# Optimization experiments

Measured on AMD Instinct MI355X. Metric: run time of the kernel, lower is better.

Reference implementation:

```python
import jax, jax.numpy as jnp
import numpy as np

N = 8192       # nodes per graph
E = 262144     # edges per graph (avg degree 32)
H = 8          # attention heads
C = 128        # hidden dim per head (H*C = 1024 to match Linear(1024,128))
IN = 128       # input feature dim
NEG_SLOPE = 0.2


def _gat_conv(x, edge_index, W, att_src, att_dst, bias):
    """PyG GATConv (concat=True, add_self_loops=True, shared lin for src/dst)."""
    n = x.shape[0]
    loop = jnp.arange(n, dtype=edge_index.dtype)
    src = jnp.concatenate([edge_index[0], loop])  # [E+N]
    dst = jnp.concatenate([edge_index[1], loop])
    h = (x @ W).reshape(n, H, C)                         # [N,H,C]
    a_src = jnp.sum(h * att_src, axis=-1)                # [N,H]
    a_dst = jnp.sum(h * att_dst, axis=-1)                # [N,H]
    e = jax.nn.leaky_relu(a_src[src] + a_dst[dst], NEG_SLOPE)   # [E+N,H]
    m = jax.ops.segment_max(e, dst, num_segments=n)      # per-dst max for stability
    ex = jnp.exp(e - m[dst])
    den = jax.ops.segment_sum(ex, dst, num_segments=n)
    alpha = ex / den[dst]                                # [E+N,H] neighborhood softmax
    out = jax.ops.segment_sum(h[src] * alpha[:, :, None], dst, num_segments=n)
    return out.reshape(n, H * C) + bias                  # [N, H*C]


def setup_inputs() -> dict:
    key = jax.random.key(0)
    ks = jax.random.split(key, 12)
    s = 0.05  # keep activations in a sane range
    return {
        "x1": jax.random.normal(ks[0], (N, IN), jnp.float32),
        "edge_index1": jax.random.randint(ks[1], (2, E), 0, N, dtype=jnp.int64),
        "W1": jax.random.normal(ks[2], (IN, H * C), jnp.float32) * s,
        "att_src1": jax.random.normal(ks[3], (H, C), jnp.float32) * s,
        "att_dst1": jax.random.normal(ks[4], (H, C), jnp.float32) * s,
        "b1": jnp.zeros((H * C,), jnp.float32),
        "x2": jax.random.normal(ks[5], (N, IN), jnp.float32),
        "edge_index2": jax.random.randint(ks[6], (2, E), 0, N, dtype=jnp.int64),
        "W2": jax.random.normal(ks[7], (IN, H * C), jnp.float32) * s,
        "att_src2": jax.random.normal(ks[8], (H, C), jnp.float32) * s,
        "att_dst2": jax.random.normal(ks[9], (H, C), jnp.float32) * s,
        "b2": jnp.zeros((H * C,), jnp.float32),
        "Wl": jax.random.normal(ks[10], (H * C, 128), jnp.float32) * s,
        "bl": jnp.zeros((128,), jnp.float32),
    }


def reference(x1, edge_index1, W1, att_src1, att_dst1, b1,
              x2, edge_index2, W2, att_src2, att_dst2, b2, Wl, bl):
    emb1 = _gat_conv(x1, edge_index1, W1, att_src1, att_dst1, b1)  # [N1,1024]
    emb2 = _gat_conv(x2, edge_index2, W2, att_src2, att_dst2, b2)  # [N2,1024]
    scores = emb1 @ emb2.T                                          # [N1,N2]
    w1 = jax.nn.softmax(scores, axis=1)
    w2 = jax.nn.softmax(scores, axis=0)
    cross1 = (w2 @ emb2) @ Wl + bl      # [N1,128]
    cross2 = (w1.T @ emb1) @ Wl + bl    # [N2,128]
    return (jnp.mean(cross1, axis=0), jnp.mean(cross2, axis=0))
```

## Files before the change

### kernel.cpp

```cpp
#include <hip/hip_runtime.h>


#define NN 8192
#define EE 262144
#define NEG 0.2f

#define BKT 128
#define RNG (NN / BKT)
#define CAP 2560
#define EB  128
#define CHK (EE / EB)

#define U_CNT   0
#define U_G     (U_CNT + 4*BKT)
#define U_MEMB  (U_G + 2048)
#define U_ZEND  (U_MEMB + 2048)
#define U_U     (U_ZEND)
#define U_ASRC  (U_U + 2*2048)
#define U_ADST  (U_ASRC + 2*NN*8)
#define U_PR    (U_ADST + 2*NN*8)
#define U_WACC  (U_PR + 2*NN*16)
#define U_BIND  (U_WACC + 2*NN*8)
#define U_BINS  (U_BIND + 2*BKT*CAP)
#define ZERO_BYTES ((size_t)U_ZEND * 4)

__global__ __launch_bounds__(256) void k_u(
    const float* __restrict__ W1, const float* __restrict__ as1, const float* __restrict__ ad1,
    const float* __restrict__ W2, const float* __restrict__ as2, const float* __restrict__ ad2,
    float* __restrict__ u) {
  int b = blockIdx.x;
  int graph = b >> 4, sd = (b >> 3) & 1, head = b & 7;
  const float* W = graph ? W2 : W1;
  const float* att = graph ? (sd ? ad2 : as2) : (sd ? ad1 : as1);
  int w = threadIdx.x >> 6, lane = threadIdx.x & 63;
  float2 av = ((const float2*)(att + head * 128))[lane];
  float* uo = u + graph * 2048 + sd * 1024 + head * 128;
#pragma unroll 4
  for (int k = w; k < 128; k += 4) {
    float2 wv = ((const float2*)(W + (size_t)k * 1024 + head * 128))[lane];
    float p = av.x * wv.x + av.y * wv.y;
    p += __shfl_xor(p, 1);  p += __shfl_xor(p, 2);  p += __shfl_xor(p, 4);
    p += __shfl_xor(p, 8);  p += __shfl_xor(p, 16); p += __shfl_xor(p, 32);
    if (lane == 0) uo[k] = p;
  }
}

__global__ __launch_bounds__(256) void k_a(
    const float* __restrict__ x1, const float* __restrict__ x2,
    const float* __restrict__ u, float* __restrict__ asrc, float* __restrict__ adst) {
  int graph = blockIdx.y;
  const float* x = graph ? x2 : x1;
  const float* ug = u + graph * 2048;
  __shared__ float xs[64][129];
  __shared__ float us[16][128];
  int t = threadIdx.x;
  for (int i = t; i < 2048; i += 256) us[i >> 7][i & 127] = ug[i];
  int n0 = blockIdx.x * 64;
  const float* xb = x + (size_t)n0 * 128;
  for (int i = t; i < 64 * 128; i += 256) xs[i >> 7][i & 127] = xb[i];
  __syncthreads();
  int nl = t & 63;
  int j0 = (t >> 6) * 4;
  float a0 = 0.f, a1 = 0.f, a2 = 0.f, a3 = 0.f;
#pragma unroll 4
  for (int k = 0; k < 128; ++k) {
    float xv = xs[nl][k];
    a0 += xv * us[j0 + 0][k];
    a1 += xv * us[j0 + 1][k];
    a2 += xv * us[j0 + 2][k];
    a3 += xv * us[j0 + 3][k];
  }
  int n = n0 + nl;
  float* outp = (j0 < 8) ? (asrc + graph * (NN * 8) + n * 8 + j0)
                         : (adst + graph * (NN * 8) + n * 8 + (j0 - 8));
  outp[0] = a0; outp[1] = a1; outp[2] = a2; outp[3] = a3;
}

__global__ __launch_bounds__(512) void k_bin(
    const int* __restrict__ ei1, const int* __restrict__ ei2,
    int* __restrict__ cnt, int* __restrict__ binD, int* __restrict__ binS) {
  int g = blockIdx.y;
  const int* ei = g ? ei2 : ei1;
  __shared__ int hD[BKT], hS[BKT], bD[BKT], bS[BKT], cD[BKT], cS[BKT];
  int t = threadIdx.x;
  for (int i = t; i < BKT; i += 512) { hD[i] = 0; hS[i] = 0; cD[i] = 0; cS[i] = 0; }
  __syncthreads();
  int e0 = blockIdx.x * CHK;
  for (int i = t; i < CHK; i += 512) {
    int s = ei[e0 + i], d = ei[EE + e0 + i];
    atomicAdd(&hD[d >> 6], 1);
    atomicAdd(&hS[s >> 6], 1);
  }
  __syncthreads();
  for (int i = t; i < BKT; i += 512) {
    bD[i] = atomicAdd(cnt + (2 * g + 0) * BKT + i, hD[i]);
    bS[i] = atomicAdd(cnt + (2 * g + 1) * BKT + i, hS[i]);
  }
  __syncthreads();
  int* bdg = binD + (size_t)g * BKT * CAP;
  int* bsg = binS + (size_t)g * BKT * CAP;
  for (int i = t; i < CHK; i += 512) {
    int s = ei[e0 + i], d = ei[EE + e0 + i];
    int kb = d >> 6;
    int p = bD[kb] + atomicAdd(&cD[kb], 1);
    bdg[kb * CAP + p] = (s << 6) | (d & 63);
    kb = s >> 6;
    p = bS[kb] + atomicAdd(&cS[kb], 1);
    bsg[kb * CAP + p] = (d << 6) | (s & 63);
  }
}

__global__ __launch_bounds__(512) void k_den_red(
    const int* __restrict__ cnt, const int* __restrict__ binD,
    const float* __restrict__ asrc, const float* __restrict__ adst,
    float* __restrict__ pr) {
  int g = blockIdx.y, b = blockIdx.x;
  int lo = b * RNG;
  const float* as = asrc + g * (NN * 8);
  const float* ad = adst + g * (NN * 8);
  float2* prg = (float2*)pr + (size_t)g * (NN * 8);
  __shared__ float den[RNG * 8];
  __shared__ float adsts[RNG * 8];
  int t = threadIdx.x;
  for (int i = t; i < RNG * 8; i += 512) {
    float avv = ad[lo * 8 + i];
    float v = as[lo * 8 + i] + avv;
    v = v > 0.f ? v : NEG * v;
    adsts[i] = avv;
    den[i] = __expf(v);
  }
  __syncthreads();
  int n = cnt[(2 * g + 0) * BKT + b];
  const int* recs = binD + (size_t)g * BKT * CAP + b * CAP;
  int rid = t >> 3, h = t & 7;
  for (int base = 0; base < n; base += 256) {
    int rv[4]; bool ok[4]; float sv[4];
#pragma unroll
    for (int uu = 0; uu < 4; ++uu) {
      int i = base + uu * 64 + rid;
      ok[uu] = i < n;
      rv[uu] = ok[uu] ? recs[i] : 0;
    }
#pragma unroll
    for (int uu = 0; uu < 4; ++uu)
      sv[uu] = ok[uu] ? as[(rv[uu] >> 6) * 8 + h] : 0.f;
#pragma unroll
    for (int uu = 0; uu < 4; ++uu) {
      if (ok[uu]) {
        int dl = rv[uu] & 63;
        float v = sv[uu] + adsts[dl * 8 + h];
        v = v > 0.f ? v : NEG * v;
        atomicAdd(&den[dl * 8 + h], __expf(v));
      }
    }
  }
  __syncthreads();
  for (int i = t; i < RNG * 8; i += 512)
    prg[lo * 8 + i] = make_float2(adsts[i], 1.0f / den[i]);
}

__global__ __launch_bounds__(512) void k_wacc_red(
    const int* __restrict__ cnt, const int* __restrict__ binS,
    const float* __restrict__ asrc, const float* __restrict__ pr,
    float* __restrict__ wacc) {
  int g = blockIdx.y, b = blockIdx.x;
  int lo = b * RNG;
  const float* as = asrc + g * (NN * 8);
  const float2* prg = (const float2*)pr + (size_t)g * (NN * 8);
  __shared__ float wv[RNG * 8];
  __shared__ float asrcs[RNG * 8];
  int t = threadIdx.x;
  for (int i = t; i < RNG * 8; i += 512) {
    float sva = as[lo * 8 + i];
    float2 f2 = prg[lo * 8 + i];
    float v = sva + f2.x;
    v = v > 0.f ? v : NEG * v;
    asrcs[i] = sva;
    wv[i] = __expf(v) * f2.y;
  }
  __syncthreads();
  int n = cnt[(2 * g + 1) * BKT + b];
  const int* recs = binS + (size_t)g * BKT * CAP + b * CAP;
  int rid = t >> 3, h = t & 7;
  for (int base = 0; base < n; base += 256) {
    int rv[4]; bool ok[4]; float2 pv[4];
#pragma unroll
    for (int uu = 0; uu < 4; ++uu) {
      int i = base + uu * 64 + rid;
      ok[uu] = i < n;
      rv[uu] = ok[uu] ? recs[i] : 0;
    }
#pragma unroll
    for (int uu = 0; uu < 4; ++uu)
      pv[uu] = ok[uu] ? prg[(size_t)(rv[uu] >> 6) * 8 + h] : make_float2(0.f, 0.f);
#pragma unroll
    for (int uu = 0; uu < 4; ++uu) {
      if (ok[uu]) {
        int sl = rv[uu] & 63;
        float v = asrcs[sl * 8 + h] + pv[uu].x;
        v = v > 0.f ? v : NEG * v;
        atomicAdd(&wv[sl * 8 + h], __expf(v) * pv[uu].y);
      }
    }
  }
  __syncthreads();
  for (int i = t; i < RNG * 8; i += 512)
    wacc[g * (NN * 8) + lo * 8 + i] = wv[i];
}

#define GCHUNK 128
__global__ __launch_bounds__(256) void k_gred(
    const float* __restrict__ x1, const float* __restrict__ x2,
    const float* __restrict__ wacc, float* __restrict__ g) {
  int graph = blockIdx.y;
  const float* x = graph ? x2 : x1;
  const float* w = wacc + graph * (NN * 8);
  float* gg = g + graph * 1024;
  int t = threadIdx.x;
  int k = t & 127;
  int h0 = (t >> 7) * 4;
  int n0 = blockIdx.x * GCHUNK;
  float a0 = 0.f, a1 = 0.f, a2 = 0.f, a3 = 0.f;
#pragma unroll 4
  for (int n = n0; n < n0 + GCHUNK; ++n) {
    float xv = x[(size_t)n * 128 + k];
    float4 wv4 = *(const float4*)(w + (size_t)n * 8 + h0);
    a0 += xv * wv4.x; a1 += xv * wv4.y; a2 += xv * wv4.z; a3 += xv * wv4.w;
  }
  atomicAdd(gg + (h0 + 0) * 128 + k, a0);
  atomicAdd(gg + (h0 + 1) * 128 + k, a1);
  atomicAdd(gg + (h0 + 2) * 128 + k, a2);
  atomicAdd(gg + (h0 + 3) * 128 + k, a3);
}

__global__ __launch_bounds__(256) void k_memb(
    const float* __restrict__ W1, const float* __restrict__ W2,
    const float* __restrict__ b1, const float* __restrict__ b2,
    const float* __restrict__ g, float* __restrict__ memb) {
  int graph = blockIdx.z;
  int kc = blockIdx.y;
  const float* W = graph ? W2 : W1;
  const float* b = graph ? b2 : b1;
  int e = blockIdx.x * 256 + threadIdx.x;
  int head = e >> 7;
  const float* gr = g + graph * 1024 + head * 128;
  float s = 0.f;
#pragma unroll
  for (int k = kc * 16; k < kc * 16 + 16; ++k) s += gr[k] * W[(size_t)k * 1024 + e];
  s *= (1.0f / (float)NN);
  if (kc == 0) s += b[e];
  atomicAdd(memb + graph * 1024 + e, s);
}

__global__ __launch_bounds__(256) void k_out(
    const float* __restrict__ memb, const float* __restrict__ Wl,
    const float* __restrict__ bl, float* __restrict__ out) {
  int t = threadIdx.x;
  int j = t & 127;
  int k0 = blockIdx.x * 32;
  const float* m = (t < 128) ? (memb + 1024) : memb;
  float s = 0.f;
#pragma unroll
  for (int k = k0; k < k0 + 32; ++k) s += m[k] * Wl[(size_t)k * 128 + j];
  if (blockIdx.x == 0) s += bl[j];
  atomicAdd(out + t, s);
}

extern "C" void kernel_launch(void* const* d_in, const int* in_sizes, int n_in,
                              void* d_out, int out_size, void* d_ws, size_t ws_size,
                              hipStream_t stream) {
  const float* x1  = (const float*)d_in[0];
  const int*   ei1 = (const int*)d_in[1];
  const float* W1  = (const float*)d_in[2];
  const float* as1 = (const float*)d_in[3];
  const float* ad1 = (const float*)d_in[4];
  const float* b1  = (const float*)d_in[5];
  const float* x2  = (const float*)d_in[6];
  const int*   ei2 = (const int*)d_in[7];
  const float* W2  = (const float*)d_in[8];
  const float* as2 = (const float*)d_in[9];
  const float* ad2 = (const float*)d_in[10];
  const float* b2  = (const float*)d_in[11];
  const float* Wl  = (const float*)d_in[12];
  const float* bl  = (const float*)d_in[13];
  float* out = (float*)d_out;

  int*   cnt  = (int*)d_ws + U_CNT;
  float* g    = (float*)d_ws + U_G;
  float* memb = (float*)d_ws + U_MEMB;
  float* u    = (float*)d_ws + U_U;
  float* asrc = (float*)d_ws + U_ASRC;
  float* adst = (float*)d_ws + U_ADST;
  float* pr   = (float*)d_ws + U_PR;
  float* wacc = (float*)d_ws + U_WACC;
  int*   binD = (int*)d_ws + U_BIND;
  int*   binS = (int*)d_ws + U_BINS;

  hipMemsetAsync(d_ws, 0, ZERO_BYTES, stream);
  hipMemsetAsync(d_out, 0, (size_t)out_size * 4, stream);

  k_bin<<<dim3(EB, 2), 512, 0, stream>>>(ei1, ei2, cnt, binD, binS);
  k_u<<<32, 256, 0, stream>>>(W1, as1, ad1, W2, as2, ad2, u);
  k_a<<<dim3(NN / 64, 2), 256, 0, stream>>>(x1, x2, u, asrc, adst);
  k_den_red<<<dim3(BKT, 2), 512, 0, stream>>>(cnt, binD, asrc, adst, pr);
  k_wacc_red<<<dim3(BKT, 2), 512, 0, stream>>>(cnt, binS, asrc, pr, wacc);
  k_gred<<<dim3(NN / GCHUNK, 2), 256, 0, stream>>>(x1, x2, wacc, g);
  k_memb<<<dim3(4, 8, 2), 256, 0, stream>>>(W1, W2, b1, b2, g, memb);
  k_out<<<32, 256, 0, stream>>>(memb, Wl, bl, out);
}
```

Measured before the change: 192.0 us.

## Fuse all stages into one persistent kernel with grid-wide barriers

Replaces the eight separate kernel launches with a single persistent kernel of 256 blocks that moves between phases through software grid barriers built on a global atomic counter. The final tiny projection is done by the last-arriving block, which removes the output memset and the separate k_out launch. The goal is to remove per-launch overhead and inter-kernel gaps in a pipeline made of many short stages. The cost is barrier spin latency, and correctness relies on all 256 blocks being resident at the same time, since a non-resident block would deadlock the barrier.

Result: slower. 429.2 us (+123.5%).

```diff
diff --git a/kernel.cpp b/kernel.cpp
--- a/kernel.cpp
+++ b/kernel.cpp
@@ -12,7 +12,8 @@
 #define CHK (EE / EB)
 
 #define U_CNT   0
-#define U_G     (U_CNT + 4*BKT)
+#define U_BAR   (U_CNT + 4*BKT + 64)
+#define U_G     (U_BAR + 16)
 #define U_MEMB  (U_G + 2048)
 #define U_ZEND  (U_MEMB + 2048)
 #define U_U     (U_ZEND)
@@ -24,246 +25,267 @@
 #define U_BINS  (U_BIND + 2*BKT*CAP)
 #define ZERO_BYTES ((size_t)U_ZEND * 4)
 
-__global__ __launch_bounds__(256) void k_u(
-    const float* __restrict__ W1, const float* __restrict__ as1, const float* __restrict__ ad1,
-    const float* __restrict__ W2, const float* __restrict__ as2, const float* __restrict__ ad2,
-    float* __restrict__ u) {
-  int b = blockIdx.x;
-  int graph = b >> 4, sd = (b >> 3) & 1, head = b & 7;
-  const float* W = graph ? W2 : W1;
-  const float* att = graph ? (sd ? ad2 : as2) : (sd ? ad1 : as1);
-  int w = threadIdx.x >> 6, lane = threadIdx.x & 63;
-  float2 av = ((const float2*)(att + head * 128))[lane];
-  float* uo = u + graph * 2048 + sd * 1024 + head * 128;
+union SMem {
+  struct { int hD[BKT]; int hS[BKT]; int bD[BKT]; int bS[BKT]; int cD[BKT]; int cS[BKT]; } bin;
+  struct { float xs[64][129]; float us[16][128]; } a;
+  struct { float den[RNG * 8]; float ad[RNG * 8]; } dr;
+  struct { float wv[RNG * 8]; float as[RNG * 8]; } wr;
+  float po[512];
+};
+
+__device__ __forceinline__ void gbar(int* bar, int target) {
+  __threadfence();
+  __syncthreads();
+  if (threadIdx.x == 0) {
+    __hip_atomic_fetch_add(bar, 1, __ATOMIC_RELAXED, __HIP_MEMORY_SCOPE_AGENT);
+    while (__hip_atomic_load(bar, __ATOMIC_RELAXED, __HIP_MEMORY_SCOPE_AGENT) < target)
+      __builtin_amdgcn_s_sleep(2);
+    __threadfence();
+  }
+  __syncthreads();
+}
+
+__global__ __launch_bounds__(512, 1) void k_fused(
+    const float* __restrict__ x1, const int* __restrict__ ei1,
+    const float* __restrict__ W1, const float* __restrict__ as1,
+    const float* __restrict__ ad1, const float* __restrict__ b1,
+    const float* __restrict__ x2, const int* __restrict__ ei2,
+    const float* __restrict__ W2, const float* __restrict__ as2,
+    const float* __restrict__ ad2, const float* __restrict__ b2,
+    const float* __restrict__ Wl, const float* __restrict__ bl,
+    int* __restrict__ cnt, int* __restrict__ bar,
+    float* __restrict__ gacc, float* __restrict__ memb,
+    float* __restrict__ u, float* __restrict__ asrc, float* __restrict__ adst,
+    float* __restrict__ pr, float* __restrict__ wacc,
+    int* __restrict__ binD, int* __restrict__ binS, float* __restrict__ out) {
+  __shared__ SMem sm;
+  __shared__ int lastF;
+  const int blk = (int)blockIdx.x;
+  const int t = (int)threadIdx.x;
+
+  if (blk >= 224) {
+    int b = blk - 224;
+    int graph = b >> 4, sd = (b >> 3) & 1, head = b & 7;
+    const float* W = graph ? W2 : W1;
+    const float* att = graph ? (sd ? ad2 : as2) : (sd ? ad1 : as1);
+    int w = t >> 6, lane = t & 63;
+    float2 av = ((const float2*)(att + head * 128))[lane];
+    float* uo = u + graph * 2048 + sd * 1024 + head * 128;
+    for (int k = w; k < 128; k += 8) {
+      float2 wv = ((const float2*)(W + (size_t)k * 1024 + head * 128))[lane];
+      float p = av.x * wv.x + av.y * wv.y;
+      p += __shfl_xor(p, 1);  p += __shfl_xor(p, 2);  p += __shfl_xor(p, 4);
+      p += __shfl_xor(p, 8);  p += __shfl_xor(p, 16); p += __shfl_xor(p, 32);
+      if (lane == 0) uo[k] = p;
+    }
+  }
+  gbar(bar, 256);
+
+  {
+    const int gph = blk >> 7;
+    const int cb = blk & 127;
+    const int* ei = gph ? ei2 : ei1;
+    for (int i = t; i < BKT; i += 512) {
+      sm.bin.hD[i] = 0; sm.bin.hS[i] = 0; sm.bin.cD[i] = 0; sm.bin.cS[i] = 0;
+    }
+    __syncthreads();
+    const int e0 = cb * CHK;
+    for (int i = t; i < CHK; i += 512) {
+      int s = ei[e0 + i], d = ei[EE + e0 + i];
+      atomicAdd(&sm.bin.hD[d >> 6], 1);
+      atomicAdd(&sm.bin.hS[s >> 6], 1);
+    }
+    __syncthreads();
+    for (int i = t; i < BKT; i += 512) {
+      sm.bin.bD[i] = atomicAdd(cnt + (2 * gph + 0) * BKT + i, sm.bin.hD[i]);
+      sm.bin.bS[i] = atomicAdd(cnt + (2 * gph + 1) * BKT + i, sm.bin.hS[i]);
+    }
+    __syncthreads();
+    int* bdg = binD + (size_t)gph * BKT * CAP;
+    int* bsg = binS + (size_t)gph * BKT * CAP;
+    for (int i = t; i < CHK; i += 512) {
+      int s = ei[e0 + i], d = ei[EE + e0 + i];
+      int kb = d >> 6;
+      int p = sm.bin.bD[kb] + atomicAdd(&sm.bin.cD[kb], 1);
+      bdg[kb * CAP + p] = (s << 6) | (d & 63);
+      kb = s >> 6;
+      p = sm.bin.bS[kb] + atomicAdd(&sm.bin.cS[kb], 1);
+      bsg[kb * CAP + p] = (d << 6) | (s & 63);
+    }
+    __syncthreads();
+
+    const float* x = gph ? x2 : x1;
+    const float* ug = u + gph * 2048;
+    for (int i = t; i < 2048; i += 512) sm.a.us[i >> 7][i & 127] = ug[i];
+    const int n0 = cb * 64;
+    const float* xb = x + (size_t)n0 * 128;
+    for (int i = t; i < 64 * 128; i += 512) sm.a.xs[i >> 7][i & 127] = xb[i];
+    __syncthreads();
+    int nl = t & 63;
+    int j0 = (t >> 6) * 2;
+    float a0 = 0.f, a1 = 0.f;
 #pragma unroll 4
-  for (int k = w; k < 128; k += 4) {
-    float2 wv = ((const float2*)(W + (size_t)k * 1024 + head * 128))[lane];
-    float p = av.x * wv.x + av.y * wv.y;
-    p += __shfl_xor(p, 1);  p += __shfl_xor(p, 2);  p += __shfl_xor(p, 4);
-    p += __shfl_xor(p, 8);  p += __shfl_xor(p, 16); p += __shfl_xor(p, 32);
-    if (lane == 0) uo[k] = p;
-  }
-}
-
-__global__ __launch_bounds__(256) void k_a(
-    const float* __restrict__ x1, const float* __restrict__ x2,
-    const float* __restrict__ u, float* __restrict__ asrc, float* __restrict__ adst) {
-  int graph = blockIdx.y;
-  const float* x = graph ? x2 : x1;
-  const float* ug = u + graph * 2048;
-  __shared__ float xs[64][129];
-  __shared__ float us[16][128];
-  int t = threadIdx.x;
-  for (int i = t; i < 2048; i += 256) us[i >> 7][i & 127] = ug[i];
-  int n0 = blockIdx.x * 64;
-  const float* xb = x + (size_t)n0 * 128;
-  for (int i = t; i < 64 * 128; i += 256) xs[i >> 7][i & 127] = xb[i];
+    for (int k = 0; k < 128; ++k) {
+      float xv = sm.a.xs[nl][k];
+      a0 += xv * sm.a.us[j0 + 0][k];
+      a1 += xv * sm.a.us[j0 + 1][k];
+    }
+    int n = n0 + nl;
+    float* outp = (j0 < 8) ? (asrc + gph * (NN * 8) + n * 8 + j0)
+                           : (adst + gph * (NN * 8) + n * 8 + (j0 - 8));
+    outp[0] = a0; outp[1] = a1;
+  }
+  gbar(bar, 512);
+
+  {
+    const int gph = blk >> 7, b = blk & 127;
+    const int lo = b * RNG;
+    const float* as = asrc + gph * (NN * 8);
+    const float* ad = adst + gph * (NN * 8);
+    float2* prg = (float2*)pr + (size_t)gph * (NN * 8);
+    for (int i = t; i < RNG * 8; i += 512) {
+      float avv = ad[lo * 8 + i];
+      float v = as[lo * 8 + i] + avv;
+      v = v > 0.f ? v : NEG * v;
+      sm.dr.ad[i] = avv;
+      sm.dr.den[i] = __expf(v);
+    }
+    __syncthreads();
+    int n = __hip_atomic_load(cnt + (2 * gph + 0) * BKT + b,
+                              __ATOMIC_RELAXED, __HIP_MEMORY_SCOPE_AGENT);
+    const int* recs = binD + (size_t)gph * BKT * CAP + b * CAP;
+    int rid = t >> 3, h = t & 7;
+    for (int base = 0; base < n; base += 256) {
+      int rv[4]; bool ok[4]; float sv[4];
+#pragma unroll
+      for (int uu = 0; uu < 4; ++uu) {
+        int i = base + uu * 64 + rid;
+        ok[uu] = i < n;
+        rv[uu] = ok[uu] ? recs[i] : 0;
+      }
+#pragma unroll
+      for (int uu = 0; uu < 4; ++uu)
+        sv[uu] = ok[uu] ? as[(rv[uu] >> 6) * 8 + h] : 0.f;
+#pragma unroll
+      for (int uu = 0; uu < 4; ++uu) {
+        if (ok[uu]) {
+          int dl = rv[uu] & 63;
+          float v = sv[uu] + sm.dr.ad[dl * 8 + h];
+          v = v > 0.f ? v : NEG * v;
+          atomicAdd(&sm.dr.den[dl * 8 + h], __expf(v));
+        }
+      }
+    }
+    __syncthreads();
+    for (int i = t; i < RNG * 8; i += 512)
+      prg[lo * 8 + i] = make_float2(sm.dr.ad[i], 1.0f / sm.dr.den[i]);
+  }
+  gbar(bar, 768);
+
+  {
+    const int gph = blk >> 7, b = blk & 127;
+    const int lo = b * RNG;
+    const float* as = asrc + gph * (NN * 8);
+    const float2* prg = (const float2*)pr + (size_t)gph * (NN * 8);
+    for (int i = t; i < RNG * 8; i += 512) {
+      float sva = as[lo * 8 + i];
+      float2 f2 = prg[lo * 8 + i];
+      float v = sva + f2.x;
+      v = v > 0.f ? v : NEG * v;
+      sm.wr.as[i] = sva;
+      sm.wr.wv[i] = __expf(v) * f2.y;
+    }
+    __syncthreads();
+    int n = __hip_atomic_load(cnt + (2 * gph + 1) * BKT + b,
+                              __ATOMIC_RELAXED, __HIP_MEMORY_SCOPE_AGENT);
+    const int* recs = binS + (size_t)gph * BKT * CAP + b * CAP;
+    int rid = t >> 3, h = t & 7;
+    for (int base = 0; base < n; base += 256) {
+      int rv[4]; bool ok[4]; float2 pv[4];
+#pragma unroll
+      for (int uu = 0; uu < 4; ++uu) {
+        int i = base + uu * 64 + rid;
+        ok[uu] = i < n;
+        rv[uu] = ok[uu] ? recs[i] : 0;
+      }
+#pragma unroll
+      for (int uu = 0; uu < 4; ++uu)
+        pv[uu] = ok[uu] ? prg[(size_t)(rv[uu] >> 6) * 8 + h] : make_float2(0.f, 0.f);
+#pragma unroll
+      for (int uu = 0; uu < 4; ++uu) {
+        if (ok[uu]) {
+          int sl = rv[uu] & 63;
+          float v = sm.wr.as[sl * 8 + h] + pv[uu].x;
+          v = v > 0.f ? v : NEG * v;
+          atomicAdd(&sm.wr.wv[sl * 8 + h], __expf(v) * pv[uu].y);
+        }
+      }
+    }
+    __syncthreads();
+    for (int i = t; i < RNG * 8; i += 512)
+      wacc[gph * (NN * 8) + lo * 8 + i] = sm.wr.wv[i];
+  }
+  gbar(bar, 1024);
+
+  {
+    const int gph = blk >> 7;
+    const float* x = gph ? x2 : x1;
+    const float* w = wacc + gph * (NN * 8);
+    float* gg = gacc + gph * 1024;
+    int k = t & 127;
+    int h0 = (t >> 7) * 2;
+    int n0 = (blk & 127) * 64;
+    float a0 = 0.f, a1 = 0.f;
+#pragma unroll 4
+    for (int n = n0; n < n0 + 64; ++n) {
+      float xv = x[(size_t)n * 128 + k];
+      float2 wv2 = *(const float2*)(w + (size_t)n * 8 + h0);
+      a0 += xv * wv2.x; a1 += xv * wv2.y;
+    }
+    atomicAdd(gg + (h0 + 0) * 128 + k, a0);
+    atomicAdd(gg + (h0 + 1) * 128 + k, a1);
+  }
+  gbar(bar, 1280);
+
+  if (blk >= 32) return;
+  {
+    int gph = blk >> 4, kc = (blk >> 1) & 7, eb = blk & 1;
+    int e = eb * 512 + t;
+    const float* W = gph ? W2 : W1;
+    const float* bb = gph ? b2 : b1;
+    int head = e >> 7;
+    const float* gr = gacc + gph * 1024 + head * 128;
+    float s = 0.f;
+#pragma unroll
+    for (int k = kc * 16; k < kc * 16 + 16; ++k) s += gr[k] * W[(size_t)k * 1024 + e];
+    s *= (1.0f / (float)NN);
+    if (kc == 0) s += bb[e];
+    atomicAdd(memb + gph * 1024 + e, s);
+  }
+  __threadfence();
   __syncthreads();
-  int nl = t & 63;
-  int j0 = (t >> 6) * 4;
-  float a0 = 0.f, a1 = 0.f, a2 = 0.f, a3 = 0.f;
-#pragma unroll 4
-  for (int k = 0; k < 128; ++k) {
-    float xv = xs[nl][k];
-    a0 += xv * us[j0 + 0][k];
-    a1 += xv * us[j0 + 1][k];
-    a2 += xv * us[j0 + 2][k];
-    a3 += xv * us[j0 + 3][k];
-  }
-  int n = n0 + nl;
-  float* outp = (j0 < 8) ? (asrc + graph * (NN * 8) + n * 8 + j0)
-                         : (adst + graph * (NN * 8) + n * 8 + (j0 - 8));
-  outp[0] = a0; outp[1] = a1; outp[2] = a2; outp[3] = a3;
-}
-
-__global__ __launch_bounds__(512) void k_bin(
-    const int* __restrict__ ei1, const int* __restrict__ ei2,
-    int* __restrict__ cnt, int* __restrict__ binD, int* __restrict__ binS) {
-  int g = blockIdx.y;
-  const int* ei = g ? ei2 : ei1;
-  __shared__ int hD[BKT], hS[BKT], bD[BKT], bS[BKT], cD[BKT], cS[BKT];
-  int t = threadIdx.x;
-  for (int i = t; i < BKT; i += 512) { hD[i] = 0; hS[i] = 0; cD[i] = 0; cS[i] = 0; }
+  if (t == 0) {
+    int prev = __hip_atomic_fetch_add(bar + 1, 1, __ATOMIC_ACQ_REL,
+                                      __HIP_MEMORY_SCOPE_AGENT);
+    lastF = (prev == 31);
+  }
   __syncthreads();
-  int e0 = blockIdx.x * CHK;
-  for (int i = t; i < CHK; i += 512) {
-    int s = ei[e0 + i], d = ei[EE + e0 + i];
-    atomicAdd(&hD[d >> 6], 1);
-    atomicAdd(&hS[s >> 6], 1);
-  }
-  __syncthreads();
-  for (int i = t; i < BKT; i += 512) {
-    bD[i] = atomicAdd(cnt + (2 * g + 0) * BKT + i, hD[i]);
-    bS[i] = atomicAdd(cnt + (2 * g + 1) * BKT + i, hS[i]);
-  }
-  __syncthreads();
-  int* bdg = binD + (size_t)g * BKT * CAP;
-  int* bsg = binS + (size_t)g * BKT * CAP;
-  for (int i = t; i < CHK; i += 512) {
-    int s = ei[e0 + i], d = ei[EE + e0 + i];
-    int kb = d >> 6;
-    int p = bD[kb] + atomicAdd(&cD[kb], 1);
-    bdg[kb * CAP + p] = (s << 6) | (d & 63);
-    kb = s >> 6;
-    p = bS[kb] + atomicAdd(&cS[kb], 1);
-    bsg[kb * CAP + p] = (d << 6) | (s & 63);
-  }
-}
-
-__global__ __launch_bounds__(512) void k_den_red(
-    const int* __restrict__ cnt, const int* __restrict__ binD,
-    const float* __restrict__ asrc, const float* __restrict__ adst,
-    float* __restrict__ pr) {
-  int g = blockIdx.y, b = blockIdx.x;
-  int lo = b * RNG;
-  const float* as = asrc + g * (NN * 8);
-  const float* ad = adst + g * (NN * 8);
-  float2* prg = (float2*)pr + (size_t)g * (NN * 8);
-  __shared__ float den[RNG * 8];
-  __shared__ float adsts[RNG * 8];
-  int t = threadIdx.x;
-  for (int i = t; i < RNG * 8; i += 512) {
-    float avv = ad[lo * 8 + i];
-    float v = as[lo * 8 + i] + avv;
-    v = v > 0.f ? v : NEG * v;
-    adsts[i] = avv;
-    den[i] = __expf(v);
-  }
-  __syncthreads();
-  int n = cnt[(2 * g + 0) * BKT + b];
-  const int* recs = binD + (size_t)g * BKT * CAP + b * CAP;
-  int rid = t >> 3, h = t & 7;
-  for (int base = 0; base < n; base += 256) {
-    int rv[4]; bool ok[4]; float sv[4];
-#pragma unroll
-    for (int uu = 0; uu < 4; ++uu) {
-      int i = base + uu * 64 + rid;
-      ok[uu] = i < n;
-      rv[uu] = ok[uu] ? recs[i] : 0;
-    }
-#pragma unroll
-    for (int uu = 0; uu < 4; ++uu)
-      sv[uu] = ok[uu] ? as[(rv[uu] >> 6) * 8 + h] : 0.f;
-#pragma unroll
-    for (int uu = 0; uu < 4; ++uu) {
-      if (ok[uu]) {
-        int dl = rv[uu] & 63;
-        float v = sv[uu] + adsts[dl * 8 + h];
-        v = v > 0.f ? v : NEG * v;
-        atomicAdd(&den[dl * 8 + h], __expf(v));
-      }
-    }
-  }
-  __syncthreads();
-  for (int i = t; i < RNG * 8; i += 512)
-    prg[lo * 8 + i] = make_float2(adsts[i], 1.0f / den[i]);
-}
-
-__global__ __launch_bounds__(512) void k_wacc_red(
-    const int* __restrict__ cnt, const int* __restrict__ binS,
-    const float* __restrict__ asrc, const float* __restrict__ pr,
-    float* __restrict__ wacc) {
-  int g = blockIdx.y, b = blockIdx.x;
-  int lo = b * RNG;
-  const float* as = asrc + g * (NN * 8);
-  const float2* prg = (const float2*)pr + (size_t)g * (NN * 8);
-  __shared__ float wv[RNG * 8];
-  __shared__ float asrcs[RNG * 8];
-  int t = threadIdx.x;
-  for (int i = t; i < RNG * 8; i += 512) {
-    float sva = as[lo * 8 + i];
-    float2 f2 = prg[lo * 8 + i];
-    float v = sva + f2.x;
-    v = v > 0.f ? v : NEG * v;
-    asrcs[i] = sva;
-    wv[i] = __expf(v) * f2.y;
-  }
-  __syncthreads();
-  int n = cnt[(2 * g + 1) * BKT + b];
-  const int* recs = binS + (size_t)g * BKT * CAP + b * CAP;
-  int rid = t >> 3, h = t & 7;
-  for (int base = 0; base < n; base += 256) {
-    int rv[4]; bool ok[4]; float2 pv[4];
-#pragma unroll
-    for (int uu = 0; uu < 4; ++uu) {
-      int i = base + uu * 64 + rid;
-      ok[uu] = i < n;
-      rv[uu] = ok[uu] ? recs[i] : 0;
-    }
-#pragma unroll
-    for (int uu = 0; uu < 4; ++uu)
-      pv[uu] = ok[uu] ? prg[(size_t)(rv[uu] >> 6) * 8 + h] : make_float2(0.f, 0.f);
-#pragma unroll
-    for (int uu = 0; uu < 4; ++uu) {
-      if (ok[uu]) {
-        int sl = rv[uu] & 63;
-        float v = asrcs[sl * 8 + h] + pv[uu].x;
-        v = v > 0.f ? v : NEG * v;
-        atomicAdd(&wv[sl * 8 + h], __expf(v) * pv[uu].y);
-      }
-    }
-  }
-  __syncthreads();
-  for (int i = t; i < RNG * 8; i += 512)
-    wacc[g * (NN * 8) + lo * 8 + i] = wv[i];
-}
-
-#define GCHUNK 128
-__global__ __launch_bounds__(256) void k_gred(
-    const float* __restrict__ x1, const float* __restrict__ x2,
-    const float* __restrict__ wacc, float* __restrict__ g) {
-  int graph = blockIdx.y;
-  const float* x = graph ? x2 : x1;
-  const float* w = wacc + graph * (NN * 8);
-  float* gg = g + graph * 1024;
-  int t = threadIdx.x;
-  int k = t & 127;
-  int h0 = (t >> 7) * 4;
-  int n0 = blockIdx.x * GCHUNK;
-  float a0 = 0.f, a1 = 0.f, a2 = 0.f, a3 = 0.f;
-#pragma unroll 4
-  for (int n = n0; n < n0 + GCHUNK; ++n) {
-    float xv = x[(size_t)n * 128 + k];
-    float4 wv4 = *(const float4*)(w + (size_t)n * 8 + h0);
-    a0 += xv * wv4.x; a1 += xv * wv4.y; a2 += xv * wv4.z; a3 += xv * wv4.w;
-  }
-  atomicAdd(gg + (h0 + 0) * 128 + k, a0);
-  atomicAdd(gg + (h0 + 1) * 128 + k, a1);
-  atomicAdd(gg + (h0 + 2) * 128 + k, a2);
-  atomicAdd(gg + (h0 + 3) * 128 + k, a3);
-}
-
-__global__ __launch_bounds__(256) void k_memb(
-    const float* __restrict__ W1, const float* __restrict__ W2,
-    const float* __restrict__ b1, const float* __restrict__ b2,
-    const float* __restrict__ g, float* __restrict__ memb) {
-  int graph = blockIdx.z;
-  int kc = blockIdx.y;
-  const float* W = graph ? W2 : W1;
-  const float* b = graph ? b2 : b1;
-  int e = blockIdx.x * 256 + threadIdx.x;
-  int head = e >> 7;
-  const float* gr = g + graph * 1024 + head * 128;
-  float s = 0.f;
-#pragma unroll
-  for (int k = kc * 16; k < kc * 16 + 16; ++k) s += gr[k] * W[(size_t)k * 1024 + e];
-  s *= (1.0f / (float)NN);
-  if (kc == 0) s += b[e];
-  atomicAdd(memb + graph * 1024 + e, s);
-}
-
-__global__ __launch_bounds__(256) void k_out(
-    const float* __restrict__ memb, const float* __restrict__ Wl,
-    const float* __restrict__ bl, float* __restrict__ out) {
-  int t = threadIdx.x;
-  int j = t & 127;
-  int k0 = blockIdx.x * 32;
-  const float* m = (t < 128) ? (memb + 1024) : memb;
-  float s = 0.f;
-#pragma unroll
-  for (int k = k0; k < k0 + 32; ++k) s += m[k] * Wl[(size_t)k * 128 + j];
-  if (blockIdx.x == 0) s += bl[j];
-  atomicAdd(out + t, s);
+  if (!lastF) return;
+  __threadfence();
+
+  {
+    int o = t & 255;
+    int kh = t >> 8;
+    int j = o & 127;
+    const float* m = (o < 128) ? (memb + 1024) : memb;
+    float s = 0.f;
+#pragma unroll 8
+    for (int k = kh * 512; k < kh * 512 + 512; ++k)
+      s += m[k] * Wl[(size_t)k * 128 + j];
+    sm.po[t] = s;
+    __syncthreads();
+    if (t < 256) out[t] = sm.po[t] + sm.po[t + 256] + bl[t & 127];
+  }
 }
 
 extern "C" void kernel_launch(void* const* d_in, const int* in_sizes, int n_in,
@@ -286,7 +308,8 @@
   float* out = (float*)d_out;
 
   int*   cnt  = (int*)d_ws + U_CNT;
-  float* g    = (float*)d_ws + U_G;
+  int*   bar  = (int*)d_ws + U_BAR;
+  float* gacc = (float*)d_ws + U_G;
   float* memb = (float*)d_ws + U_MEMB;
   float* u    = (float*)d_ws + U_U;
   float* asrc = (float*)d_ws + U_ASRC;
@@ -297,14 +320,8 @@
   int*   binS = (int*)d_ws + U_BINS;
 
   hipMemsetAsync(d_ws, 0, ZERO_BYTES, stream);
-  hipMemsetAsync(d_out, 0, (size_t)out_size * 4, stream);
-
-  k_bin<<<dim3(EB, 2), 512, 0, stream>>>(ei1, ei2, cnt, binD, binS);
-  k_u<<<32, 256, 0, stream>>>(W1, as1, ad1, W2, as2, ad2, u);
-  k_a<<<dim3(NN / 64, 2), 256, 0, stream>>>(x1, x2, u, asrc, adst);
-  k_den_red<<<dim3(BKT, 2), 512, 0, stream>>>(cnt, binD, asrc, adst, pr);
-  k_wacc_red<<<dim3(BKT, 2), 512, 0, stream>>>(cnt, binS, asrc, pr, wacc);
-  k_gred<<<dim3(NN / GCHUNK, 2), 256, 0, stream>>>(x1, x2, wacc, g);
-  k_memb<<<dim3(4, 8, 2), 256, 0, stream>>>(W1, W2, b1, b2, g, memb);
-  k_out<<<32, 256, 0, stream>>>(memb, Wl, bl, out);
+
+  k_fused<<<256, 512, 0, stream>>>(
+      x1, ei1, W1, as1, ad1, b1, x2, ei2, W2, as2, ad2, b2, Wl, bl,
+      cnt, bar, gacc, memb, u, asrc, adst, pr, wacc, binD, binS, out);
 }
```
